# Performance work log

Measured on AMD Instinct MI355X. Metric: run time of the kernel, lower is better.

## Reference

```python
import jax, jax.numpy as jnp
import numpy as np

N = 100000      # nodes
E = 1600000     # edges (avg degree 16)
IN = 128        # in_channels
H = 128         # hidden_channels
OUT = 64        # out_channels
NHID = 3        # num_layers (hidden->hidden SAGE convs)


def _lin(k, fan_out, fan_in):
    s = 1.0 / np.sqrt(fan_in)
    return jax.random.uniform(k, (fan_out, fan_in), jnp.float32, -s, s)


def setup_inputs() -> dict:
    key = jax.random.key(0)
    ks = jax.random.split(key, 12)
    x = jax.random.normal(ks[0], (N, IN), dtype=jnp.float32)
    edge_index = jax.random.randint(ks[1], (2, E), 0, N, dtype=jnp.int32)
    # inProj Linear(IN -> H)
    Wp = _lin(ks[2], H, IN)
    bp = jnp.zeros((H,), jnp.float32)
    # 3 hidden SAGEConv(H -> H): lin_l (with bias) on aggregated neighbors, lin_r (no bias) on root
    Wl_h = jnp.stack([_lin(jax.random.fold_in(ks[3], i), H, H) for i in range(NHID)])
    bl_h = jnp.zeros((NHID, H), jnp.float32)
    Wr_h = jnp.stack([_lin(jax.random.fold_in(ks[4], i), H, H) for i in range(NHID)])
    # output SAGEConv(H -> OUT)
    Wl_o = _lin(ks[5], OUT, H)
    bl_o = jnp.zeros((OUT,), jnp.float32)
    Wr_o = _lin(ks[6], OUT, H)
    return {"x": x, "edge_index": edge_index, "Wp": Wp, "bp": bp,
            "Wl_h": Wl_h, "bl_h": bl_h, "Wr_h": Wr_h,
            "Wl_o": Wl_o, "bl_o": bl_o, "Wr_o": Wr_o}


def reference(x, edge_index, Wp, bp, Wl_h, bl_h, Wr_h, Wl_o, bl_o, Wr_o):
    src, dst = edge_index[0], edge_index[1]
    ones = jnp.ones((E,), x.dtype)
    deg = jax.ops.segment_sum(ones, dst, num_segments=N)           # [N]
    inv_deg = (1.0 / jnp.maximum(deg, 1.0))[:, None]               # [N,1]

    def sage(h, Wl, bl, Wr):
        # mean aggregation of source features onto destinations (irregular gather+scatter)
        s = jax.ops.segment_sum(h[src], dst, num_segments=N)       # [N,d]
        mean = s * inv_deg
        return mean @ Wl.T + bl + h @ Wr.T

    h = x @ Wp.T + bp
    inp = h
    h = jax.nn.relu(h)
    for i in range(NHID):
        h = sage(h, Wl_h[i], bl_h[i], Wr_h[i])
        h = jax.nn.relu(h)                                          # dropout is identity in eval
        h = h + 0.2 * inp
    h = sage(h, Wl_o, bl_o, Wr_o)
    return jax.nn.log_softmax(h, axis=-1)
```

## Files before the change

### kernel.cpp

```cpp
#include <hip/hip_runtime.h>
#include <math.h>

#define N_NODES 100000
#define N_EDGES 1600000
#define NBUK 391
#define PCHUNK 8192
#define NPBLK 196

typedef unsigned short u16;
typedef unsigned char u8;
typedef __bf16 bf16x8 __attribute__((ext_vector_type(8)));
typedef float f32x4 __attribute__((ext_vector_type(4)));
typedef float f32x2 __attribute__((ext_vector_type(2)));

#define OFF_RP      0u
#define OFF_INVDEG  400016u
#define OFF_BHIST   800016u
#define OFF_BBASE   801600u
#define OFF_GCUR    803200u
#define OFF_PAIRS   804800u
#define OFF_COL     13604800u
#define OFF_PACK    20004800u
#define OFF_INP     20266944u
#define OFF_H       45866944u
#define OFF_H8A     71466944u
#define OFF_H8B     84266944u
#define OFF_GL      97066944u
#define OFF_GR      109866944u
#define OFF_MEAN    122666944u
#define WS_NEEDED   148266944u

#define PK_WP   0
#define PK_WL   16384
#define PK_WR   65536
#define PK_WLO  114688
#define PK_WRO  122880

__device__ __forceinline__ float bfl(unsigned u) {
  union { unsigned i; float f; } v; v.i = u << 16; return v.f;
}
__device__ __forceinline__ float bfh(unsigned u) {
  union { unsigned i; float f; } v; v.i = u & 0xFFFF0000u; return v.f;
}
__device__ __forceinline__ u16 f2b(float f) {
  union { float f; unsigned i; } v; v.f = f;
  unsigned r = (v.i + 0x7FFFu + ((v.i >> 16) & 1u)) >> 16;
  return (u16)r;
}

__global__ __launch_bounds__(256) void pack_weights_k(
    const float* __restrict__ Wp, const float* __restrict__ Wl,
    const float* __restrict__ Wr, const float* __restrict__ Wlo,
    const float* __restrict__ Wro, u16* __restrict__ P) {
  int t = blockIdx.x * 256 + threadIdx.x;
  if (t >= 16384) return;
  const float* W; u16* dst; int j; int NT;
  if (t < 2048)        { W = Wp;                    dst = P + PK_WP;                j = t;                 NT = 8; }
  else if (t < 8192)   { int m = (t - 2048) >> 11;  j = (t - 2048) & 2047;
                         W = Wl + (m << 14);        dst = P + PK_WL + (m << 14);    NT = 8; }
  else if (t < 14336)  { int m = (t - 8192) >> 11;  j = (t - 8192) & 2047;
                         W = Wr + (m << 14);        dst = P + PK_WR + (m << 14);    NT = 8; }
  else if (t < 15360)  { j = t - 14336;             W = Wlo;  dst = P + PK_WLO;     NT = 4; }
  else                 { j = t - 15360;             W = Wro;  dst = P + PK_WRO;     NT = 4; }
  int lane = j & 63;
  int nt, kt;
  if (NT == 8) { nt = (j >> 6) & 7; kt = j >> 9; }
  else         { nt = (j >> 6) & 3; kt = j >> 8; }
  int n  = nt * 16 + (lane & 15);
  int k0 = kt * 32 + ((lane >> 4) << 3);
  const float* s = W + n * 128 + k0;
  ushort4 lo = make_ushort4(f2b(s[0]), f2b(s[1]), f2b(s[2]), f2b(s[3]));
  ushort4 hi = make_ushort4(f2b(s[4]), f2b(s[5]), f2b(s[6]), f2b(s[7]));
  *(ushort4*)(dst + j * 8)     = lo;
  *(ushort4*)(dst + j * 8 + 4) = hi;
}

__global__ __launch_bounds__(256) void bhist_k(const int* __restrict__ dst,
                                               int* __restrict__ bhist) {
  __shared__ int lc[NBUK];
  int t = threadIdx.x;
  for (int i = t; i < NBUK; i += 256) lc[i] = 0;
  __syncthreads();
  int base = blockIdx.x * 4096;
#pragma unroll
  for (int r = 0; r < 16; r++) {
    int i = base + r * 256 + t;
    if (i < N_EDGES) atomicAdd(&lc[dst[i] >> 8], 1);
  }
  __syncthreads();
  for (int i = t; i < NBUK; i += 256)
    if (lc[i]) atomicAdd(&bhist[i], lc[i]);
}

__global__ __launch_bounds__(512) void bscan_k(const int* __restrict__ bhist,
                                               int* __restrict__ bbase,
                                               int* __restrict__ gcur,
                                               int* __restrict__ rp) {
  __shared__ int s[512];
  int t = threadIdx.x;
  int v = (t < NBUK) ? bhist[t] : 0;
  s[t] = v;
  __syncthreads();
  for (int off = 1; off < 512; off <<= 1) {
    int u = (t >= off) ? s[t - off] : 0;
    __syncthreads();
    s[t] += u;
    __syncthreads();
  }
  if (t < NBUK) { int e = s[t] - v; bbase[t] = e; gcur[t] = e; }
  if (t == NBUK - 1) { bbase[NBUK] = s[t]; rp[N_NODES] = s[t]; }
}

__global__ __launch_bounds__(256) void part_k(const int* __restrict__ src,
                                              const int* __restrict__ dst,
                                              int* __restrict__ gcur,
                                              uint2* __restrict__ pairs) {
  __shared__ int lcnt[NBUK + 1];
  __shared__ int lofs[512];
  __shared__ int cur[NBUK];
  __shared__ int gslot[NBUK];
  __shared__ uint2 stag[PCHUNK];
  int t = threadIdx.x;
  for (int i = t; i < NBUK + 1; i += 256) lcnt[i] = 0;
  __syncthreads();
  int base = blockIdx.x * PCHUNK;
#pragma unroll
  for (int r = 0; r < PCHUNK / 256; r++) {
    int i = base + r * 256 + t;
    if (i < N_EDGES) atomicAdd(&lcnt[dst[i] >> 8], 1);
  }
  __syncthreads();
  {
    int e1 = t + 256;
    lofs[t]  = (t  <= NBUK) ? lcnt[t]  : 0;
    lofs[e1] = (e1 <= NBUK) ? lcnt[e1] : 0;
    __syncthreads();
    for (int off = 1; off < 512; off <<= 1) {
      int a0 = (t  >= off) ? lofs[t  - off] : 0;
      int a1 = (e1 >= off) ? lofs[e1 - off] : 0;
      __syncthreads();
      lofs[t] += a0; lofs[e1] += a1;
      __syncthreads();
    }
    int o0 = lofs[t]  - ((t  <= NBUK) ? lcnt[t]  : 0);
    int o1 = lofs[e1] - ((e1 <= NBUK) ? lcnt[e1] : 0);
    __syncthreads();
    lofs[t] = o0; lofs[e1] = o1;
    __syncthreads();
  }
  for (int i = t; i < NBUK; i += 256) cur[i] = lofs[i];
  __syncthreads();
#pragma unroll
  for (int r = 0; r < PCHUNK / 256; r++) {
    int i = base + r * 256 + t;
    if (i < N_EDGES) {
      int d = dst[i];
      int slot = atomicAdd(&cur[d >> 8], 1);
      stag[slot] = make_uint2((unsigned)src[i], (unsigned)d);
    }
  }
  __syncthreads();
  for (int i = t; i < NBUK; i += 256)
    if (lcnt[i]) gslot[i] = atomicAdd(&gcur[i], lcnt[i]);
  __syncthreads();
  int total = lofs[NBUK];
  for (int p = t; p < total; p += 256) {
    uint2 pr = stag[p];
    int b = (int)(pr.y >> 8);
    pairs[gslot[b] + (p - lofs[b])] = pr;
  }
}

__global__ __launch_bounds__(256) void csr_k(const uint2* __restrict__ pairs,
                                             const int* __restrict__ bbase,
                                             int* __restrict__ rp,
                                             float* __restrict__ invdeg,
                                             int* __restrict__ col) {
  __shared__ int cnt[256];
  __shared__ int scn[256];
  __shared__ int cur[256];
  int b = blockIdx.x, t = threadIdx.x;
  int lo = bbase[b], hi = bbase[b + 1];
  cnt[t] = 0;
  __syncthreads();
  for (int p = lo + t; p < hi; p += 256)
    atomicAdd(&cnt[pairs[p].y & 255], 1);
  __syncthreads();
  int c = cnt[t];
  scn[t] = c;
  __syncthreads();
  for (int off = 1; off < 256; off <<= 1) {
    int v = (t >= off) ? scn[t - off] : 0;
    __syncthreads();
    scn[t] += v;
    __syncthreads();
  }
  int excl = scn[t] - c;
  int node = (b << 8) + t;
  if (node < N_NODES) {
    rp[node] = lo + excl;
    invdeg[node] = 1.0f / (float)(c > 1 ? c : 1);
  }
  cur[t] = lo + excl;
  __syncthreads();
  for (int p = lo + t; p < hi; p += 256) {
    uint2 pr = pairs[p];
    int slot = atomicAdd(&cur[pr.y & 255], 1);
    col[slot] = (int)pr.x;
  }
}

__global__ __launch_bounds__(256) void aggregate_fp8_k(const u8* __restrict__ h8,
                                                       const int* __restrict__ rp,
                                                       const int* __restrict__ col,
                                                       const float* __restrict__ invdeg,
                                                       u16* __restrict__ mean) {
  int node = blockIdx.x * 8 + (threadIdx.x >> 5);
  int lane = threadIdx.x & 31;
  if (node >= N_NODES) return;
  int beg = rp[node], end = rp[node + 1];
  const u8* hp = h8 + lane * 4;
  float a0 = 0.f, a1 = 0.f, a2 = 0.f, a3 = 0.f;
  int j = beg;
  for (; j + 3 < end; j += 4) {
    int s0 = col[j], s1 = col[j + 1], s2 = col[j + 2], s3 = col[j + 3];
    unsigned v0 = *(const unsigned*)(hp + ((long)s0 << 7));
    unsigned v1 = *(const unsigned*)(hp + ((long)s1 << 7));
    unsigned v2 = *(const unsigned*)(hp + ((long)s2 << 7));
    unsigned v3 = *(const unsigned*)(hp + ((long)s3 << 7));
    f32x2 p0 = __builtin_amdgcn_cvt_pk_f32_fp8(v0, false);
    f32x2 p1 = __builtin_amdgcn_cvt_pk_f32_fp8(v0, true);
    f32x2 p2 = __builtin_amdgcn_cvt_pk_f32_fp8(v1, false);
    f32x2 p3 = __builtin_amdgcn_cvt_pk_f32_fp8(v1, true);
    f32x2 p4 = __builtin_amdgcn_cvt_pk_f32_fp8(v2, false);
    f32x2 p5 = __builtin_amdgcn_cvt_pk_f32_fp8(v2, true);
    f32x2 p6 = __builtin_amdgcn_cvt_pk_f32_fp8(v3, false);
    f32x2 p7 = __builtin_amdgcn_cvt_pk_f32_fp8(v3, true);
    a0 += (p0[0] + p2[0]) + (p4[0] + p6[0]);
    a1 += (p0[1] + p2[1]) + (p4[1] + p6[1]);
    a2 += (p1[0] + p3[0]) + (p5[0] + p7[0]);
    a3 += (p1[1] + p3[1]) + (p5[1] + p7[1]);
  }
  for (; j < end; j++) {
    unsigned v0 = *(const unsigned*)(hp + ((long)col[j] << 7));
    f32x2 p0 = __builtin_amdgcn_cvt_pk_f32_fp8(v0, false);
    f32x2 p1 = __builtin_amdgcn_cvt_pk_f32_fp8(v0, true);
    a0 += p0[0]; a1 += p0[1]; a2 += p1[0]; a3 += p1[1];
  }
  float wd = invdeg[node];
  *(ushort4*)(mean + ((long)node << 7) + lane * 4) =
      make_ushort4(f2b(a0 * wd), f2b(a1 * wd), f2b(a2 * wd), f2b(a3 * wd));
}

__global__ __launch_bounds__(256) void inproj_mfma_k(
    const float* __restrict__ X, const u16* __restrict__ P,
    const float* __restrict__ bias,
    u16* __restrict__ inp, u16* __restrict__ hout, u8* __restrict__ h8out, int M) {
  __shared__ float zb[64 * 132];
  int tid = threadIdx.x;
  int w = tid >> 6, lane = tid & 63;
  int quad = lane >> 4, l15 = lane & 15;
  int m0 = blockIdx.x * 64;
  int rowa = m0 + w * 16 + l15; if (rowa > M - 1) rowa = M - 1;
  f32x4 acc[8] = {};
#pragma unroll
  for (int kt = 0; kt < 4; kt++) {
    const float* xr = X + (long)rowa * 128 + kt * 32 + quad * 8;
    float4 p0 = *(const float4*)xr;
    float4 p1 = *(const float4*)(xr + 4);
    union { ushort4 u4[2]; bf16x8 v; } fa;
    fa.u4[0] = make_ushort4(f2b(p0.x), f2b(p0.y), f2b(p0.z), f2b(p0.w));
    fa.u4[1] = make_ushort4(f2b(p1.x), f2b(p1.y), f2b(p1.z), f2b(p1.w));
    const u16* pb = P + ((kt * 8) * 64 + lane) * 8;
#pragma unroll
    for (int nt = 0; nt < 8; nt++) {
      bf16x8 bf = *(const bf16x8*)(pb + nt * 512);
      acc[nt] = __builtin_amdgcn_mfma_f32_16x16x32_bf16(fa.v, bf, acc[nt], 0, 0, 0);
    }
  }
#pragma unroll
  for (int nt = 0; nt < 8; nt++) {
    int c = nt * 16 + l15;
    float b = bias[c];
#pragma unroll
    for (int r = 0; r < 4; r++)
      zb[(w * 16 + quad * 4 + r) * 132 + c] = acc[nt][r] + b;
  }
  __syncthreads();
  int r = lane >> 2, seg = lane & 3;
  long grow = m0 + w * 16 + r;
  if (grow < M) {
    const float* zrow = &zb[(w * 16 + r) * 132 + seg * 32];
    u16* ip = inp + grow * 128 + seg * 32;
    u16* hp = hout + grow * 128 + seg * 32;
    u8*  qp = h8out + grow * 128 + seg * 32;
#pragma unroll
    for (int b = 0; b < 4; b++) {
      float zv[8];
      *(float4*)&zv[0] = *(const float4*)(zrow + b * 8);
      *(float4*)&zv[4] = *(const float4*)(zrow + b * 8 + 4);
      float rv[8];
#pragma unroll
      for (int jj = 0; jj < 8; jj++) rv[jj] = fmaxf(zv[jj], 0.f);
      *(ushort4*)(ip + b * 8)     = make_ushort4(f2b(zv[0]), f2b(zv[1]), f2b(zv[2]), f2b(zv[3]));
      *(ushort4*)(ip + b * 8 + 4) = make_ushort4(f2b(zv[4]), f2b(zv[5]), f2b(zv[6]), f2b(zv[7]));
      *(ushort4*)(hp + b * 8)     = make_ushort4(f2b(rv[0]), f2b(rv[1]), f2b(rv[2]), f2b(rv[3]));
      *(ushort4*)(hp + b * 8 + 4) = make_ushort4(f2b(rv[4]), f2b(rv[5]), f2b(rv[6]), f2b(rv[7]));
      unsigned q0 = 0, q1 = 0;
      q0 = __builtin_amdgcn_cvt_pk_fp8_f32(rv[0], rv[1], q0, false);
      q0 = __builtin_amdgcn_cvt_pk_fp8_f32(rv[2], rv[3], q0, true);
      q1 = __builtin_amdgcn_cvt_pk_fp8_f32(rv[4], rv[5], q1, false);
      q1 = __builtin_amdgcn_cvt_pk_fp8_f32(rv[6], rv[7], q1, true);
      *(uint2*)(qp + b * 8) = make_uint2(q0, q1);
    }
  }
}

__global__ __launch_bounds__(256) void sage_mfma8_k(
    const u16* __restrict__ A0, const u16* __restrict__ P0,
    const u16* __restrict__ A1, const u16* __restrict__ P1,
    const float* __restrict__ bias, const u16* __restrict__ inp,
    u16* __restrict__ outp, u8* __restrict__ h8out, int M) {
  __shared__ float zb[64 * 132];
  int tid = threadIdx.x;
  int w = tid >> 6, lane = tid & 63;
  int quad = lane >> 4, l15 = lane & 15;
  int m0 = blockIdx.x * 64;
  int rowa = m0 + w * 16 + l15; if (rowa > M - 1) rowa = M - 1;
  f32x4 acc[8] = {};
#pragma unroll
  for (int kt = 0; kt < 4; kt++) {
    bf16x8 am = *(const bf16x8*)(A0 + (long)rowa * 128 + kt * 32 + quad * 8);
    bf16x8 ar = *(const bf16x8*)(A1 + (long)rowa * 128 + kt * 32 + quad * 8);
    const u16* pl = P0 + ((kt * 8) * 64 + lane) * 8;
    const u16* pr = P1 + ((kt * 8) * 64 + lane) * 8;
#pragma unroll
    for (int nt = 0; nt < 8; nt++) {
      bf16x8 b0 = *(const bf16x8*)(pl + nt * 512);
      bf16x8 b1 = *(const bf16x8*)(pr + nt * 512);
      acc[nt] = __builtin_amdgcn_mfma_f32_16x16x32_bf16(am, b0, acc[nt], 0, 0, 0);
      acc[nt] = __builtin_amdgcn_mfma_f32_16x16x32_bf16(ar, b1, acc[nt], 0, 0, 0);
    }
  }
#pragma unroll
  for (int nt = 0; nt < 8; nt++) {
    int c = nt * 16 + l15;
    float b = bias[c];
#pragma unroll
    for (int r = 0; r < 4; r++)
      zb[(w * 16 + quad * 4 + r) * 132 + c] = fmaxf(acc[nt][r] + b, 0.f);
  }
  __syncthreads();
  int r = lane >> 2, seg = lane & 3;
  long grow = m0 + w * 16 + r;
  if (grow < M) {
    const float* zrow = &zb[(w * 16 + r) * 132 + seg * 32];
    const u16* ip = inp + grow * 128 + seg * 32;
    u16* op = outp + grow * 128 + seg * 32;
#pragma unroll
    for (int b = 0; b < 4; b++) {
      float zv[8];
      *(float4*)&zv[0] = *(const float4*)(zrow + b * 8);
      *(float4*)&zv[4] = *(const float4*)(zrow + b * 8 + 4);
      uint2 iv0 = *(const uint2*)(ip + b * 8);
      uint2 iv1 = *(const uint2*)(ip + b * 8 + 4);
      float fv[8];
      fv[0] = zv[0] + 0.2f * bfl(iv0.x); fv[1] = zv[1] + 0.2f * bfh(iv0.x);
      fv[2] = zv[2] + 0.2f * bfl(iv0.y); fv[3] = zv[3] + 0.2f * bfh(iv0.y);
      fv[4] = zv[4] + 0.2f * bfl(iv1.x); fv[5] = zv[5] + 0.2f * bfh(iv1.x);
      fv[6] = zv[6] + 0.2f * bfl(iv1.y); fv[7] = zv[7] + 0.2f * bfh(iv1.y);
      *(ushort4*)(op + b * 8)     = make_ushort4(f2b(fv[0]), f2b(fv[1]), f2b(fv[2]), f2b(fv[3]));
      *(ushort4*)(op + b * 8 + 4) = make_ushort4(f2b(fv[4]), f2b(fv[5]), f2b(fv[6]), f2b(fv[7]));
      if (h8out) {
        unsigned q0 = 0, q1 = 0;
        q0 = __builtin_amdgcn_cvt_pk_fp8_f32(fv[0], fv[1], q0, false);
        q0 = __builtin_amdgcn_cvt_pk_fp8_f32(fv[2], fv[3], q0, true);
        q1 = __builtin_amdgcn_cvt_pk_fp8_f32(fv[4], fv[5], q1, false);
        q1 = __builtin_amdgcn_cvt_pk_fp8_f32(fv[6], fv[7], q1, true);
        *(uint2*)(h8out + grow * 128 + seg * 32 + b * 8) = make_uint2(q0, q1);
      }
    }
  }
}

__global__ __launch_bounds__(256) void out_proj_k(
    const u16* __restrict__ A, const u16* __restrict__ PLO,
    const u16* __restrict__ PRO, u16* __restrict__ gl, u16* __restrict__ gr, int M) {
  __shared__ float zb[64 * 132];
  int tid = threadIdx.x;
  int w = tid >> 6, lane = tid & 63;
  int quad = lane >> 4, l15 = lane & 15;
  int m0 = blockIdx.x * 64;
  int rowa = m0 + w * 16 + l15; if (rowa > M - 1) rowa = M - 1;
  f32x4 acc[8] = {};
#pragma unroll
  for (int kt = 0; kt < 4; kt++) {
    bf16x8 af = *(const bf16x8*)(A + (long)rowa * 128 + kt * 32 + quad * 8);
#pragma unroll
    for (int nt = 0; nt < 4; nt++) {
      bf16x8 b0 = *(const bf16x8*)(PLO + ((kt * 4 + nt) * 64 + lane) * 8);
      bf16x8 b1 = *(const bf16x8*)(PRO + ((kt * 4 + nt) * 64 + lane) * 8);
      acc[nt]     = __builtin_amdgcn_mfma_f32_16x16x32_bf16(af, b0, acc[nt], 0, 0, 0);
      acc[4 + nt] = __builtin_amdgcn_mfma_f32_16x16x32_bf16(af, b1, acc[4 + nt], 0, 0, 0);
    }
  }
#pragma unroll
  for (int nt = 0; nt < 4; nt++) {
    int c = nt * 16 + l15;
#pragma unroll
    for (int r = 0; r < 4; r++) {
      zb[(w * 16 + quad * 4 + r) * 132 + c]      = acc[nt][r];
      zb[(w * 16 + quad * 4 + r) * 132 + 64 + c] = acc[4 + nt][r];
    }
  }
  __syncthreads();
  int r = lane >> 2, seg = lane & 3;
  long grow = m0 + w * 16 + r;
  if (grow < M) {
    const float* zrow = &zb[(w * 16 + r) * 132 + seg * 32];
    u16* dp = (seg < 2) ? (gl + grow * 64 + seg * 32) : (gr + grow * 64 + (seg - 2) * 32);
#pragma unroll
    for (int b = 0; b < 4; b++) {
      float zv[8];
      *(float4*)&zv[0] = *(const float4*)(zrow + b * 8);
      *(float4*)&zv[4] = *(const float4*)(zrow + b * 8 + 4);
      *(ushort4*)(dp + b * 8)     = make_ushort4(f2b(zv[0]), f2b(zv[1]), f2b(zv[2]), f2b(zv[3]));
      *(ushort4*)(dp + b * 8 + 4) = make_ushort4(f2b(zv[4]), f2b(zv[5]), f2b(zv[6]), f2b(zv[7]));
    }
  }
}

__global__ __launch_bounds__(256) void out_final_k(
    const u16* __restrict__ gl, const u16* __restrict__ gr,
    const float* __restrict__ blo, const int* __restrict__ rp,
    const int* __restrict__ col, const float* __restrict__ invdeg,
    float* __restrict__ outp) {
  int node = blockIdx.x * 8 + (threadIdx.x >> 5);
  int lane = threadIdx.x & 31;
  if (node >= N_NODES) return;
  int beg = rp[node], end = rp[node + 1];
  const u16* glp = gl + lane * 2;
  float a0 = 0.f, a1 = 0.f;
  int j = beg;
  for (; j + 3 < end; j += 4) {
    int s0 = col[j], s1 = col[j + 1], s2 = col[j + 2], s3 = col[j + 3];
    unsigned v0 = *(const unsigned*)(glp + ((long)s0 << 6));
    unsigned v1 = *(const unsigned*)(glp + ((long)s1 << 6));
    unsigned v2 = *(const unsigned*)(glp + ((long)s2 << 6));
    unsigned v3 = *(const unsigned*)(glp + ((long)s3 << 6));
    a0 += (bfl(v0) + bfl(v1)) + (bfl(v2) + bfl(v3));
    a1 += (bfh(v0) + bfh(v1)) + (bfh(v2) + bfh(v3));
  }
  for (; j < end; j++) {
    unsigned v0 = *(const unsigned*)(glp + ((long)col[j] << 6));
    a0 += bfl(v0); a1 += bfh(v0);
  }
  float wd = invdeg[node];
  unsigned g = *(const unsigned*)(gr + (long)node * 64 + lane * 2);
  float z0 = a0 * wd + bfl(g) + blo[lane * 2];
  float z1 = a1 * wd + bfh(g) + blo[lane * 2 + 1];
  float mx = fmaxf(z0, z1);
#pragma unroll
  for (int off = 16; off >= 1; off >>= 1) mx = fmaxf(mx, __shfl_xor(mx, off, 32));
  float s = __expf(z0 - mx) + __expf(z1 - mx);
#pragma unroll
  for (int off = 16; off >= 1; off >>= 1) s += __shfl_xor(s, off, 32);
  float ro = mx + __logf(s);
  float2 o = make_float2(z0 - ro, z1 - ro);
  *(float2*)(outp + (long)node * 64 + lane * 2) = o;
}

extern "C" void kernel_launch(void* const* d_in, const int* in_sizes, int n_in,
                              void* d_out, int out_size, void* d_ws, size_t ws_size,
                              hipStream_t stream) {
  if (ws_size < (size_t)WS_NEEDED) return;
  const float* x   = (const float*)d_in[0];
  const int*   ei  = (const int*)d_in[1];
  const float* Wp  = (const float*)d_in[2];
  const float* bp  = (const float*)d_in[3];
  const float* Wl  = (const float*)d_in[4];
  const float* bl  = (const float*)d_in[5];
  const float* Wr  = (const float*)d_in[6];
  const float* Wlo = (const float*)d_in[7];
  const float* blo = (const float*)d_in[8];
  const float* Wro = (const float*)d_in[9];
  float* out = (float*)d_out;
  char* ws = (char*)d_ws;
  int*   rp     = (int*)(ws + OFF_RP);
  float* invdeg = (float*)(ws + OFF_INVDEG);
  int*   bhist  = (int*)(ws + OFF_BHIST);
  int*   bbase  = (int*)(ws + OFF_BBASE);
  int*   gcur   = (int*)(ws + OFF_GCUR);
  uint2* pairs  = (uint2*)(ws + OFF_PAIRS);
  int*   col    = (int*)(ws + OFF_COL);
  u16*   pack   = (u16*)(ws + OFF_PACK);
  u16*   inp    = (u16*)(ws + OFF_INP);
  u16*   h      = (u16*)(ws + OFF_H);
  u8*    h8a    = (u8*)(ws + OFF_H8A);
  u8*    h8b    = (u8*)(ws + OFF_H8B);
  u16*   gl     = (u16*)(ws + OFF_GL);
  u16*   gr     = (u16*)(ws + OFF_GR);
  u16*   mean   = (u16*)(ws + OFF_MEAN);
  const int* srcv = ei;
  const int* dstv = ei + N_EDGES;

  hipMemsetAsync(ws + OFF_BHIST, 0, (NBUK + 1) * 4, stream);
  pack_weights_k<<<64, 256, 0, stream>>>(Wp, Wl, Wr, Wlo, Wro, pack);
  bhist_k<<<391, 256, 0, stream>>>(dstv, bhist);
  bscan_k<<<1, 512, 0, stream>>>(bhist, bbase, gcur, rp);
  part_k<<<NPBLK, 256, 0, stream>>>(srcv, dstv, gcur, pairs);
  csr_k<<<NBUK, 256, 0, stream>>>(pairs, bbase, rp, invdeg, col);

  int gblk = (N_NODES + 63) / 64;
  int fblk = (N_NODES + 7) / 8;

  inproj_mfma_k<<<gblk, 256, 0, stream>>>(x, pack + PK_WP, bp, inp, h, h8a, N_NODES);

  aggregate_fp8_k<<<fblk, 256, 0, stream>>>(h8a, rp, col, invdeg, mean);
  sage_mfma8_k<<<gblk, 256, 0, stream>>>(mean, pack + PK_WL, h, pack + PK_WR,
                                         bl, inp, h, h8b, N_NODES);
  aggregate_fp8_k<<<fblk, 256, 0, stream>>>(h8b, rp, col, invdeg, mean);
  sage_mfma8_k<<<gblk, 256, 0, stream>>>(mean, pack + PK_WL + 16384, h, pack + PK_WR + 16384,
                                         bl + 128, inp, h, h8a, N_NODES);
  aggregate_fp8_k<<<fblk, 256, 0, stream>>>(h8a, rp, col, invdeg, mean);
  sage_mfma8_k<<<gblk, 256, 0, stream>>>(mean, pack + PK_WL + 32768, h, pack + PK_WR + 32768,
                                         bl + 256, inp, h, (u8*)nullptr, N_NODES);

  out_proj_k<<<gblk, 256, 0, stream>>>(h, pack + PK_WLO, pack + PK_WRO, gl, gr, N_NODES);
  out_final_k<<<fblk, 256, 0, stream>>>(gl, gr, blo, rp, col, invdeg, out);
}
```

Before: 546.8 us.

## Split gathered features into column planes with XCC-affine persistent gather kernels

Stores the fp8 hidden features and the output-projection gather input as four column planes (32 bytes or 16 bf16 per node per plane) rather than full rows. New persistent gather kernels pick a starting plane from the hardware XCC id and take node chunks from atomic counters, so each XCD mostly works on one plane. The intent is to keep each plane's random-gather working set small enough to hit in that XCD's L2 instead of missing to memory. The output layer is split into a plane gather that writes fp32 partials and a separate log-softmax kernel. This adds an extra pass and intermediate buffer, atomic scheduling overhead, and 32-byte gathers that are less efficient per transaction.

```diff
diff --git a/kernel.cpp b/kernel.cpp
--- a/kernel.cpp
+++ b/kernel.cpp
@@ -6,6 +6,7 @@
 #define NBUK 391
 #define PCHUNK 8192
 #define NPBLK 196
+#define CHN 64
 
 typedef unsigned short u16;
 typedef unsigned char u8;
@@ -18,17 +19,18 @@
 #define OFF_BHIST   800016u
 #define OFF_BBASE   801600u
 #define OFF_GCUR    803200u
-#define OFF_PAIRS   804800u
-#define OFF_COL     13604800u
-#define OFF_PACK    20004800u
-#define OFF_INP     20266944u
-#define OFF_H       45866944u
-#define OFF_H8A     71466944u
-#define OFF_H8B     84266944u
-#define OFF_GL      97066944u
-#define OFF_GR      109866944u
-#define OFF_MEAN    122666944u
-#define WS_NEEDED   148266944u
+#define OFF_PCTR    804800u
+#define OFF_PAIRS   805056u
+#define OFF_COL     13605056u
+#define OFF_PACK    20005056u
+#define OFF_INP     20267200u
+#define OFF_H       45867200u
+#define OFF_H8A     71467200u
+#define OFF_H8B     84267200u
+#define OFF_GL      97067200u
+#define OFF_GR      109867200u
+#define OFF_MEAN    122667200u
+#define WS_NEEDED   148267200u
 
 #define PK_WP   0
 #define PK_WL   16384
@@ -210,46 +212,128 @@
   }
 }
 
-__global__ __launch_bounds__(256) void aggregate_fp8_k(const u8* __restrict__ h8,
-                                                       const int* __restrict__ rp,
-                                                       const int* __restrict__ col,
-                                                       const float* __restrict__ invdeg,
-                                                       u16* __restrict__ mean) {
+__global__ __launch_bounds__(256) void aggregate_plane_k(
+    const u8* __restrict__ h8, const int* __restrict__ rp,
+    const int* __restrict__ col, const float* __restrict__ invdeg,
+    int* __restrict__ ctr, u16* __restrict__ mean) {
+  __shared__ int sChunk;
+  int tid = threadIdx.x;
+  int grp = tid >> 3, lane8 = tid & 7;
+  int xcc;
+  asm volatile("s_getreg_b32 %0, hwreg(HW_REG_XCC_ID)" : "=s"(xcc));
+  int myplane = (xcc >> 1) & 3;
+  for (int pp = 0; pp < 4; pp++) {
+    int pl = (myplane + pp) & 3;
+    const u8* hp = h8 + (size_t)pl * (N_NODES * 32) + lane8 * 4;
+    u16* mp = mean + (size_t)pl * (N_NODES * 32);
+    while (true) {
+      __syncthreads();
+      if (tid == 0) sChunk = atomicAdd(&ctr[pl], 1);
+      __syncthreads();
+      int base = sChunk * CHN;
+      if (base >= N_NODES) break;
+      int lim = base + CHN; if (lim > N_NODES) lim = N_NODES;
+      for (int n = base + grp; n < lim; n += 32) {
+        int beg = rp[n], end = rp[n + 1];
+        float a0 = 0.f, a1 = 0.f, a2 = 0.f, a3 = 0.f;
+        int j = beg;
+        for (; j + 3 < end; j += 4) {
+          int s0 = col[j], s1 = col[j + 1], s2 = col[j + 2], s3 = col[j + 3];
+          unsigned v0 = *(const unsigned*)(hp + (size_t)s0 * 32);
+          unsigned v1 = *(const unsigned*)(hp + (size_t)s1 * 32);
+          unsigned v2 = *(const unsigned*)(hp + (size_t)s2 * 32);
+          unsigned v3 = *(const unsigned*)(hp + (size_t)s3 * 32);
+          f32x2 p0 = __builtin_amdgcn_cvt_pk_f32_fp8(v0, false);
+          f32x2 p1 = __builtin_amdgcn_cvt_pk_f32_fp8(v0, true);
+          f32x2 p2 = __builtin_amdgcn_cvt_pk_f32_fp8(v1, false);
+          f32x2 p3 = __builtin_amdgcn_cvt_pk_f32_fp8(v1, true);
+          f32x2 p4 = __builtin_amdgcn_cvt_pk_f32_fp8(v2, false);
+          f32x2 p5 = __builtin_amdgcn_cvt_pk_f32_fp8(v2, true);
+          f32x2 p6 = __builtin_amdgcn_cvt_pk_f32_fp8(v3, false);
+          f32x2 p7 = __builtin_amdgcn_cvt_pk_f32_fp8(v3, true);
+          a0 += (p0[0] + p2[0]) + (p4[0] + p6[0]);
+          a1 += (p0[1] + p2[1]) + (p4[1] + p6[1]);
+          a2 += (p1[0] + p3[0]) + (p5[0] + p7[0]);
+          a3 += (p1[1] + p3[1]) + (p5[1] + p7[1]);
+        }
+        for (; j < end; j++) {
+          unsigned v0 = *(const unsigned*)(hp + (size_t)col[j] * 32);
+          f32x2 p0 = __builtin_amdgcn_cvt_pk_f32_fp8(v0, false);
+          f32x2 p1 = __builtin_amdgcn_cvt_pk_f32_fp8(v0, true);
+          a0 += p0[0]; a1 += p0[1]; a2 += p1[0]; a3 += p1[1];
+        }
+        float wd = invdeg[n];
+        *(ushort4*)(mp + (size_t)n * 32 + lane8 * 4) =
+            make_ushort4(f2b(a0 * wd), f2b(a1 * wd), f2b(a2 * wd), f2b(a3 * wd));
+      }
+    }
+  }
+}
+
+__global__ __launch_bounds__(256) void out_gather_k(
+    const u16* __restrict__ gl, const int* __restrict__ rp,
+    const int* __restrict__ col, const float* __restrict__ invdeg,
+    int* __restrict__ ctr, float* __restrict__ partial) {
+  __shared__ int sChunk;
+  int tid = threadIdx.x;
+  int grp = tid >> 3, lane8 = tid & 7;
+  int xcc;
+  asm volatile("s_getreg_b32 %0, hwreg(HW_REG_XCC_ID)" : "=s"(xcc));
+  int myplane = (xcc >> 1) & 3;
+  for (int pp = 0; pp < 4; pp++) {
+    int pl = (myplane + pp) & 3;
+    const u16* gp = gl + (size_t)pl * (N_NODES * 16) + lane8 * 2;
+    while (true) {
+      __syncthreads();
+      if (tid == 0) sChunk = atomicAdd(&ctr[pl], 1);
+      __syncthreads();
+      int base = sChunk * CHN;
+      if (base >= N_NODES) break;
+      int lim = base + CHN; if (lim > N_NODES) lim = N_NODES;
+      for (int n = base + grp; n < lim; n += 32) {
+        int beg = rp[n], end = rp[n + 1];
+        float a0 = 0.f, a1 = 0.f;
+        int j = beg;
+        for (; j + 3 < end; j += 4) {
+          int s0 = col[j], s1 = col[j + 1], s2 = col[j + 2], s3 = col[j + 3];
+          unsigned v0 = *(const unsigned*)(gp + (size_t)s0 * 16);
+          unsigned v1 = *(const unsigned*)(gp + (size_t)s1 * 16);
+          unsigned v2 = *(const unsigned*)(gp + (size_t)s2 * 16);
+          unsigned v3 = *(const unsigned*)(gp + (size_t)s3 * 16);
+          a0 += (bfl(v0) + bfl(v1)) + (bfl(v2) + bfl(v3));
+          a1 += (bfh(v0) + bfh(v1)) + (bfh(v2) + bfh(v3));
+        }
+        for (; j < end; j++) {
+          unsigned v0 = *(const unsigned*)(gp + (size_t)col[j] * 16);
+          a0 += bfl(v0); a1 += bfh(v0);
+        }
+        float wd = invdeg[n];
+        *(float2*)(partial + (size_t)n * 64 + pl * 16 + lane8 * 2) =
+            make_float2(a0 * wd, a1 * wd);
+      }
+    }
+  }
+}
+
+__global__ __launch_bounds__(256) void out_softmax_k(
+    const float* __restrict__ partial, const u16* __restrict__ gr,
+    const float* __restrict__ blo, float* __restrict__ outp) {
   int node = blockIdx.x * 8 + (threadIdx.x >> 5);
   int lane = threadIdx.x & 31;
   if (node >= N_NODES) return;
-  int beg = rp[node], end = rp[node + 1];
-  const u8* hp = h8 + lane * 4;
-  float a0 = 0.f, a1 = 0.f, a2 = 0.f, a3 = 0.f;
-  int j = beg;
-  for (; j + 3 < end; j += 4) {
-    int s0 = col[j], s1 = col[j + 1], s2 = col[j + 2], s3 = col[j + 3];
-    unsigned v0 = *(const unsigned*)(hp + ((long)s0 << 7));
-    unsigned v1 = *(const unsigned*)(hp + ((long)s1 << 7));
-    unsigned v2 = *(const unsigned*)(hp + ((long)s2 << 7));
-    unsigned v3 = *(const unsigned*)(hp + ((long)s3 << 7));
-    f32x2 p0 = __builtin_amdgcn_cvt_pk_f32_fp8(v0, false);
-    f32x2 p1 = __builtin_amdgcn_cvt_pk_f32_fp8(v0, true);
-    f32x2 p2 = __builtin_amdgcn_cvt_pk_f32_fp8(v1, false);
-    f32x2 p3 = __builtin_amdgcn_cvt_pk_f32_fp8(v1, true);
-    f32x2 p4 = __builtin_amdgcn_cvt_pk_f32_fp8(v2, false);
-    f32x2 p5 = __builtin_amdgcn_cvt_pk_f32_fp8(v2, true);
-    f32x2 p6 = __builtin_amdgcn_cvt_pk_f32_fp8(v3, false);
-    f32x2 p7 = __builtin_amdgcn_cvt_pk_f32_fp8(v3, true);
-    a0 += (p0[0] + p2[0]) + (p4[0] + p6[0]);
-    a1 += (p0[1] + p2[1]) + (p4[1] + p6[1]);
-    a2 += (p1[0] + p3[0]) + (p5[0] + p7[0]);
-    a3 += (p1[1] + p3[1]) + (p5[1] + p7[1]);
-  }
-  for (; j < end; j++) {
-    unsigned v0 = *(const unsigned*)(hp + ((long)col[j] << 7));
-    f32x2 p0 = __builtin_amdgcn_cvt_pk_f32_fp8(v0, false);
-    f32x2 p1 = __builtin_amdgcn_cvt_pk_f32_fp8(v0, true);
-    a0 += p0[0]; a1 += p0[1]; a2 += p1[0]; a3 += p1[1];
-  }
-  float wd = invdeg[node];
-  *(ushort4*)(mean + ((long)node << 7) + lane * 4) =
-      make_ushort4(f2b(a0 * wd), f2b(a1 * wd), f2b(a2 * wd), f2b(a3 * wd));
+  float2 pz = *(const float2*)(partial + (size_t)node * 64 + lane * 2);
+  unsigned g = *(const unsigned*)(gr + (size_t)node * 64 + lane * 2);
+  float z0 = pz.x + bfl(g) + blo[lane * 2];
+  float z1 = pz.y + bfh(g) + blo[lane * 2 + 1];
+  float mx = fmaxf(z0, z1);
+#pragma unroll
+  for (int off = 16; off >= 1; off >>= 1) mx = fmaxf(mx, __shfl_xor(mx, off, 32));
+  float s = __expf(z0 - mx) + __expf(z1 - mx);
+#pragma unroll
+  for (int off = 16; off >= 1; off >>= 1) s += __shfl_xor(s, off, 32);
+  float ro = mx + __logf(s);
+  float2 o = make_float2(z0 - ro, z1 - ro);
+  *(float2*)(outp + (size_t)node * 64 + lane * 2) = o;
 }
 
 __global__ __launch_bounds__(256) void inproj_mfma_k(
@@ -293,7 +377,7 @@
     const float* zrow = &zb[(w * 16 + r) * 132 + seg * 32];
     u16* ip = inp + grow * 128 + seg * 32;
     u16* hp = hout + grow * 128 + seg * 32;
-    u8*  qp = h8out + grow * 128 + seg * 32;
+    u8*  qp = h8out + (size_t)seg * (N_NODES * 32) + grow * 32;
 #pragma unroll
     for (int b = 0; b < 4; b++) {
       float zv[8];
@@ -330,7 +414,7 @@
   f32x4 acc[8] = {};
 #pragma unroll
   for (int kt = 0; kt < 4; kt++) {
-    bf16x8 am = *(const bf16x8*)(A0 + (long)rowa * 128 + kt * 32 + quad * 8);
+    bf16x8 am = *(const bf16x8*)(A0 + (size_t)kt * (N_NODES * 32) + (size_t)rowa * 32 + quad * 8);
     bf16x8 ar = *(const bf16x8*)(A1 + (long)rowa * 128 + kt * 32 + quad * 8);
     const u16* pl = P0 + ((kt * 8) * 64 + lane) * 8;
     const u16* pr = P1 + ((kt * 8) * 64 + lane) * 8;
@@ -377,7 +461,7 @@
         q0 = __builtin_amdgcn_cvt_pk_fp8_f32(fv[2], fv[3], q0, true);
         q1 = __builtin_amdgcn_cvt_pk_fp8_f32(fv[4], fv[5], q1, false);
         q1 = __builtin_amdgcn_cvt_pk_fp8_f32(fv[6], fv[7], q1, true);
-        *(uint2*)(h8out + grow * 128 + seg * 32 + b * 8) = make_uint2(q0, q1);
+        *(uint2*)(h8out + (size_t)seg * (N_NODES * 32) + grow * 32 + b * 8) = make_uint2(q0, q1);
       }
     }
   }
@@ -418,56 +502,22 @@
   long grow = m0 + w * 16 + r;
   if (grow < M) {
     const float* zrow = &zb[(w * 16 + r) * 132 + seg * 32];
-    u16* dp = (seg < 2) ? (gl + grow * 64 + seg * 32) : (gr + grow * 64 + (seg - 2) * 32);
 #pragma unroll
     for (int b = 0; b < 4; b++) {
       float zv[8];
       *(float4*)&zv[0] = *(const float4*)(zrow + b * 8);
       *(float4*)&zv[4] = *(const float4*)(zrow + b * 8 + 4);
-      *(ushort4*)(dp + b * 8)     = make_ushort4(f2b(zv[0]), f2b(zv[1]), f2b(zv[2]), f2b(zv[3]));
-      *(ushort4*)(dp + b * 8 + 4) = make_ushort4(f2b(zv[4]), f2b(zv[5]), f2b(zv[6]), f2b(zv[7]));
-    }
-  }
-}
-
-__global__ __launch_bounds__(256) void out_final_k(
-    const u16* __restrict__ gl, const u16* __restrict__ gr,
-    const float* __restrict__ blo, const int* __restrict__ rp,
-    const int* __restrict__ col, const float* __restrict__ invdeg,
-    float* __restrict__ outp) {
-  int node = blockIdx.x * 8 + (threadIdx.x >> 5);
-  int lane = threadIdx.x & 31;
-  if (node >= N_NODES) return;
-  int beg = rp[node], end = rp[node + 1];
-  const u16* glp = gl + lane * 2;
-  float a0 = 0.f, a1 = 0.f;
-  int j = beg;
-  for (; j + 3 < end; j += 4) {
-    int s0 = col[j], s1 = col[j + 1], s2 = col[j + 2], s3 = col[j + 3];
-    unsigned v0 = *(const unsigned*)(glp + ((long)s0 << 6));
-    unsigned v1 = *(const unsigned*)(glp + ((long)s1 << 6));
-    unsigned v2 = *(const unsigned*)(glp + ((long)s2 << 6));
-    unsigned v3 = *(const unsigned*)(glp + ((long)s3 << 6));
-    a0 += (bfl(v0) + bfl(v1)) + (bfl(v2) + bfl(v3));
-    a1 += (bfh(v0) + bfh(v1)) + (bfh(v2) + bfh(v3));
-  }
-  for (; j < end; j++) {
-    unsigned v0 = *(const unsigned*)(glp + ((long)col[j] << 6));
-    a0 += bfl(v0); a1 += bfh(v0);
-  }
-  float wd = invdeg[node];
-  unsigned g = *(const unsigned*)(gr + (long)node * 64 + lane * 2);
-  float z0 = a0 * wd + bfl(g) + blo[lane * 2];
-  float z1 = a1 * wd + bfh(g) + blo[lane * 2 + 1];
-  float mx = fmaxf(z0, z1);
-#pragma unroll
-  for (int off = 16; off >= 1; off >>= 1) mx = fmaxf(mx, __shfl_xor(mx, off, 32));
-  float s = __expf(z0 - mx) + __expf(z1 - mx);
-#pragma unroll
-  for (int off = 16; off >= 1; off >>= 1) s += __shfl_xor(s, off, 32);
-  float ro = mx + __logf(s);
-  float2 o = make_float2(z0 - ro, z1 - ro);
-  *(float2*)(outp + (long)node * 64 + lane * 2) = o;
+      u16* dp;
+      if (seg < 2) {
+        int plane = seg * 2 + (b >> 1);
+        dp = gl + (size_t)plane * (N_NODES * 16) + grow * 16 + (b & 1) * 8;
+      } else {
+        dp = gr + grow * 64 + (seg - 2) * 32 + b * 8;
+      }
+      *(ushort4*)(dp)     = make_ushort4(f2b(zv[0]), f2b(zv[1]), f2b(zv[2]), f2b(zv[3]));
+      *(ushort4*)(dp + 4) = make_ushort4(f2b(zv[4]), f2b(zv[5]), f2b(zv[6]), f2b(zv[7]));
+    }
+  }
 }
 
 extern "C" void kernel_launch(void* const* d_in, const int* in_sizes, int n_in,
@@ -491,6 +541,7 @@
   int*   bhist  = (int*)(ws + OFF_BHIST);
   int*   bbase  = (int*)(ws + OFF_BBASE);
   int*   gcur   = (int*)(ws + OFF_GCUR);
+  int*   pctr   = (int*)(ws + OFF_PCTR);
   uint2* pairs  = (uint2*)(ws + OFF_PAIRS);
   int*   col    = (int*)(ws + OFF_COL);
   u16*   pack   = (u16*)(ws + OFF_PACK);
@@ -501,10 +552,11 @@
   u16*   gl     = (u16*)(ws + OFF_GL);
   u16*   gr     = (u16*)(ws + OFF_GR);
   u16*   mean   = (u16*)(ws + OFF_MEAN);
+  float* partial = (float*)(ws + OFF_MEAN);
   const int* srcv = ei;
   const int* dstv = ei + N_EDGES;
 
-  hipMemsetAsync(ws + OFF_BHIST, 0, (NBUK + 1) * 4, stream);
+  hipMemsetAsync(ws + OFF_BHIST, 0, OFF_PAIRS - OFF_BHIST, stream);
   pack_weights_k<<<64, 256, 0, stream>>>(Wp, Wl, Wr, Wlo, Wro, pack);
   bhist_k<<<391, 256, 0, stream>>>(dstv, bhist);
   bscan_k<<<1, 512, 0, stream>>>(bhist, bbase, gcur, rp);
@@ -516,16 +568,17 @@
 
   inproj_mfma_k<<<gblk, 256, 0, stream>>>(x, pack + PK_WP, bp, inp, h, h8a, N_NODES);
 
-  aggregate_fp8_k<<<fblk, 256, 0, stream>>>(h8a, rp, col, invdeg, mean);
+  aggregate_plane_k<<<1024, 256, 0, stream>>>(h8a, rp, col, invdeg, pctr + 0, mean);
   sage_mfma8_k<<<gblk, 256, 0, stream>>>(mean, pack + PK_WL, h, pack + PK_WR,
                                          bl, inp, h, h8b, N_NODES);
-  aggregate_fp8_k<<<fblk, 256, 0, stream>>>(h8b, rp, col, invdeg, mean);
+  aggregate_plane_k<<<1024, 256, 0, stream>>>(h8b, rp, col, invdeg, pctr + 4, mean);
   sage_mfma8_k<<<gblk, 256, 0, stream>>>(mean, pack + PK_WL + 16384, h, pack + PK_WR + 16384,
                                          bl + 128, inp, h, h8a, N_NODES);
-  aggregate_fp8_k<<<fblk, 256, 0, stream>>>(h8a, rp, col, invdeg, mean);
+  aggregate_plane_k<<<1024, 256, 0, stream>>>(h8a, rp, col, invdeg, pctr + 8, mean);
   sage_mfma8_k<<<gblk, 256, 0, stream>>>(mean, pack + PK_WL + 32768, h, pack + PK_WR + 32768,
                                          bl + 256, inp, h, (u8*)nullptr, N_NODES);
 
   out_proj_k<<<gblk, 256, 0, stream>>>(h, pack + PK_WLO, pack + PK_WRO, gl, gr, N_NODES);
-  out_final_k<<<fblk, 256, 0, stream>>>(gl, gr, blo, rp, col, invdeg, out);
-}
+  out_gather_k<<<1024, 256, 0, stream>>>(gl, rp, col, invdeg, pctr + 12, partial);
+  out_softmax_k<<<fblk, 256, 0, stream>>>(partial, gr, blo, out);
+}
```

Measured after the change: 877.7 us. 1.61x slower.
